# Kernel tuning notes

Measured on AMD Instinct MI355X. Metric: run time of the kernel, lower is better.

Reference implementation:

```python
import jax, jax.numpy as jnp
import numpy as np

EMBED_DIM = 1024
N_HEADS = 16
HEAD_DIM = EMBED_DIM // N_HEADS
B, S = 2, 2048


def setup_inputs() -> dict:
    key = jax.random.key(0)
    ks = jax.random.split(key, 8)
    scale = 1.0 / np.sqrt(EMBED_DIM)
    return {
        "key": jax.random.normal(ks[0], (B, S, EMBED_DIM), jnp.float32),
        "query": jax.random.normal(ks[1], (B, S, EMBED_DIM), jnp.float32),
        "value": jax.random.normal(ks[2], (B, S, EMBED_DIM), jnp.float32),
        # nn.Linear weights stored [out_features, in_features], applied as x @ W.T
        "Wq": jax.random.normal(ks[3], (EMBED_DIM, EMBED_DIM), jnp.float32) * scale,
        "Wk": jax.random.normal(ks[4], (EMBED_DIM, EMBED_DIM), jnp.float32) * scale,
        "Wv": jax.random.normal(ks[5], (EMBED_DIM, EMBED_DIM), jnp.float32) * scale,
        "Wo": jax.random.normal(ks[6], (EMBED_DIM, EMBED_DIM), jnp.float32) * scale,
        "bo": jax.random.normal(ks[7], (EMBED_DIM,), jnp.float32) * scale,
    }


def reference(key, query, value, Wq, Wk, Wv, Wo, bo) -> jnp.ndarray:
    b = key.shape[0]
    # project and split heads: [B, S, E] -> [B, H, S, D]
    def split_heads(x):
        return x.reshape(b, -1, N_HEADS, HEAD_DIM).transpose(0, 2, 1, 3)
    q = split_heads(query @ Wq.T)
    k = split_heads(key @ Wk.T)
    v = split_heads(value @ Wv.T)
    scores = jnp.einsum("bhqd,bhkd->bhqk", q, k) / np.sqrt(HEAD_DIM)
    attn = jax.nn.softmax(scores, axis=-1)
    ctx = jnp.einsum("bhqk,bhkd->bhqd", attn, v)  # [B, H, S, D]
    ctx = ctx.transpose(0, 2, 1, 3).reshape(b, -1, EMBED_DIM)
    return ctx @ Wo.T + bo
```

## Files before the change

kernel.cpp:

```cpp
#include <hip/hip_runtime.h>

typedef unsigned short u16;
typedef __bf16 bf8 __attribute__((ext_vector_type(8)));
typedef float f4 __attribute__((ext_vector_type(4)));

typedef __attribute__((address_space(1))) const unsigned int gas_u32;
typedef __attribute__((address_space(3))) unsigned int las_u32;
#define ASYNC16(g, l) __builtin_amdgcn_global_load_lds((gas_u32*)(g), (las_u32*)(l), 16, 0, 0)

__device__ __forceinline__ u16 f2bf(float f) {
    union { float f; unsigned int u; } v; v.f = f;
    return (u16)((v.u + 0x7fffu + ((v.u >> 16) & 1u)) >> 16);
}

__device__ __forceinline__ float fexp2(float x) {
#if __has_builtin(__builtin_amdgcn_exp2f)
  return __builtin_amdgcn_exp2f(x);
#else
  return __expf(x * 0.69314718056f);
#endif
}

__global__ __launch_bounds__(256) void cvt_all(
    const float* __restrict__ k_, const float* __restrict__ q_, const float* __restrict__ v_,
    const float* __restrict__ wq, const float* __restrict__ wk, const float* __restrict__ wv,
    const float* __restrict__ wo, u16* __restrict__ ws) {
  size_t e = ((size_t)blockIdx.x * 256 + threadIdx.x) * 8;
  const float* src;
  if      (e <  4194304) src = k_ + e;
  else if (e <  8388608) src = q_ + (e - 4194304);
  else if (e < 12582912) src = v_ + (e - 8388608);
  else if (e < 13631488) src = wq + (e - 12582912);
  else if (e < 14680064) src = wk + (e - 13631488);
  else if (e < 15728640) src = wv + (e - 14680064);
  else                   src = wo + (e - 15728640);
  float4 f0 = ((const float4*)src)[0];
  float4 f1 = ((const float4*)src)[1];
  uint4 o;
  o.x = (unsigned)f2bf(f0.x) | ((unsigned)f2bf(f0.y) << 16);
  o.y = (unsigned)f2bf(f0.z) | ((unsigned)f2bf(f0.w) << 16);
  o.z = (unsigned)f2bf(f1.x) | ((unsigned)f2bf(f1.y) << 16);
  o.w = (unsigned)f2bf(f1.z) | ((unsigned)f2bf(f1.w) << 16);
  *(uint4*)(ws + e) = o;
}

template<int BM, bool FINAL>
__device__ __forceinline__ void gemm_tile(const u16* __restrict__ A, const u16* __restrict__ Bm,
                                          u16* __restrict__ Cb, float* __restrict__ Cf,
                                          const float* __restrict__ bias, float scale,
                                          int bm, int bn, int ldc) {
  __shared__ u16 As[BM*32];
  __shared__ u16 Bs[128*32];
  const int tid = threadIdx.x;
  const int wave = tid >> 6, lane = tid & 63;
  const int wm = wave >> 1, wn = wave & 1;
  const int quad = lane >> 4, l16 = lane & 15;
  const int MI = BM / 32;

  f4 acc[MI][4];
  const f4 zz = {0.f, 0.f, 0.f, 0.f};
  #pragma unroll
  for (int i = 0; i < MI; i++)
    #pragma unroll
    for (int j = 0; j < 4; j++) acc[i][j] = zz;

  const u16* ga = A  + (size_t)(bm*BM  + wave*16 + (lane>>2)) * 1024 + (lane&3)*8;
  const u16* gb = Bm + (size_t)(bn*128 + wave*16 + (lane>>2)) * 1024 + (lane&3)*8;
  u16* la = As + wave*512 + lane*8;
  u16* lb = Bs + wave*512 + lane*8;

  for (int kt = 0; kt < 1024; kt += 32) {
    ASYNC16(ga, la);
    if (BM == 128) ASYNC16(ga + 64*1024, la + 2048);
    ASYNC16(gb,           lb);
    ASYNC16(gb + 64*1024, lb + 2048);
    ga += 32; gb += 32;
    __syncthreads();
    bf8 af[MI];
    #pragma unroll
    for (int mi = 0; mi < MI; mi++)
      af[mi] = *(const bf8*)(As + (wm*(BM/2) + mi*16 + l16)*32 + quad*8);
    #pragma unroll
    for (int ni = 0; ni < 4; ni++) {
      bf8 bfr = *(const bf8*)(Bs + (wn*64 + ni*16 + l16)*32 + quad*8);
      #pragma unroll
      for (int mi = 0; mi < MI; mi++)
        acc[mi][ni] = __builtin_amdgcn_mfma_f32_16x16x32_bf16(af[mi], bfr, acc[mi][ni], 0, 0, 0);
    }
    __syncthreads();
  }

  #pragma unroll
  for (int mi = 0; mi < MI; mi++)
    #pragma unroll
    for (int ni = 0; ni < 4; ni++) {
      const int col = bn*128 + wn*64 + ni*16 + l16;
      #pragma unroll
      for (int r = 0; r < 4; r++) {
        const int row = bm*BM + wm*(BM/2) + mi*16 + quad*4 + r;
        if (FINAL) Cf[(size_t)row*ldc + col] = acc[mi][ni][r] + bias[col];
        else       Cb[(size_t)row*ldc + col] = f2bf(acc[mi][ni][r] * scale);
      }
    }
}

#define QSCALE 0.180336880f

__global__ __launch_bounds__(256, 3) void gemm_qkv(
    const u16* __restrict__ xq, const u16* __restrict__ xk, const u16* __restrict__ xv,
    const u16* __restrict__ wq, const u16* __restrict__ wk, const u16* __restrict__ wv,
    u16* __restrict__ Qo, u16* __restrict__ Ko, u16* __restrict__ Vto) {
  if (blockIdx.z == 0)
    gemm_tile<128,false>(xq, wq, Qo, nullptr, nullptr, QSCALE, blockIdx.y, blockIdx.x, 1024);
  else if (blockIdx.z == 1)
    gemm_tile<128,false>(xk, wk, Ko, nullptr, nullptr, 1.0f, blockIdx.y, blockIdx.x, 1024);
  else
    gemm_tile<128,false>(wv, xv, Vto, nullptr, nullptr, 1.0f, blockIdx.x, blockIdx.y, 4096);
}

__global__ __launch_bounds__(256, 2) void gemm_out(
    const u16* __restrict__ ctx, const u16* __restrict__ wo,
    const float* __restrict__ bias, float* __restrict__ out) {
  gemm_tile<64,true>(ctx, wo, nullptr, out, bias, 1.0f, blockIdx.y, blockIdx.x, 1024);
}

__global__ __launch_bounds__(256, 3) void flash_attn(
    const u16* __restrict__ Qg, const u16* __restrict__ Kg,
    const u16* __restrict__ Vtg, u16* __restrict__ ctx) {
  __shared__ uint4 smem4[2560];
  u16* Ks = (u16*)smem4;
  u16* Vt = (u16*)smem4 + 8192;
  u16* Pt = (u16*)smem4 + 16384;
  float* Of = (float*)smem4;
  float* Lf = (float*)smem4 + 2*64*68;

  const int tid = threadIdx.x;
  const int wave = tid >> 6, lane = tid & 63;
  const int quad = lane >> 4, l16 = lane & 15;
  const int wq = wave >> 1, wk = wave & 1;
  const int qt = blockIdx.x, h = blockIdx.y, b = blockIdx.z;
  u16* Ptw = Pt + wave*1024;

  bf8 qf[2][2];
  {
    const u16* qp = Qg + (size_t)(b*2048 + qt*64 + wq*32)*1024 + h*64;
    #pragma unroll
    for (int qs = 0; qs < 2; qs++)
      #pragma unroll
      for (int kc = 0; kc < 2; kc++)
        qf[qs][kc] = *(const bf8*)(qp + (size_t)(qs*16 + l16)*1024 + kc*32 + quad*8);
  }

  const f4 zz = {0.f, 0.f, 0.f, 0.f};
  f4 ot[4][2];
  float lrow[2] = {0.f, 0.f};
  #pragma unroll
  for (int ds = 0; ds < 4; ds++)
    #pragma unroll
    for (int qs = 0; qs < 2; qs++) ot[ds][qs] = zz;

  const int kr = tid >> 3;
  const u16* kga = Kg + (size_t)(b*2048 + kr)*1024 + h*64 + ((tid & 7) ^ (kr & 7))*8;
  const int vd = tid >> 4;
  const u16* vga = Vtg + (size_t)(h*64 + vd)*4096 + b*2048 + (((tid & 15) ^ vd))*8;
  u16* kld = Ks + tid*8;
  u16* vld = Vt + tid*8;

  for (int kv0 = 0; kv0 < 2048; kv0 += 128) {
    __syncthreads();
    #pragma unroll
    for (int p = 0; p < 4; p++) ASYNC16(kga + (size_t)(kv0 + p*32)*1024, kld + p*2048);
    #pragma unroll
    for (int p = 0; p < 4; p++) ASYNC16(vga + (size_t)(p*16)*4096 + kv0, vld + p*2048);
    __syncthreads();

    #pragma unroll
    for (int kb = 0; kb < 2; kb++) {
      f4 st[2][2];
      #pragma unroll
      for (int ks = 0; ks < 2; ks++)
        #pragma unroll
        for (int qs = 0; qs < 2; qs++) st[ks][qs] = zz;
      #pragma unroll
      for (int ks = 0; ks < 2; ks++) {
        const int key = wk*64 + kb*32 + ks*16 + l16;
        #pragma unroll
        for (int kc = 0; kc < 2; kc++) {
          bf8 kf = *(const bf8*)(Ks + key*64 + (((kc*4 + quad) ^ (l16 & 7))*8));
          #pragma unroll
          for (int qs = 0; qs < 2; qs++)
            st[ks][qs] = __builtin_amdgcn_mfma_f32_16x16x32_bf16(kf, qf[qs][kc], st[ks][qs], 0, 0, 0);
        }
      }
      #pragma unroll
      for (int ks = 0; ks < 2; ks++)
        #pragma unroll
        for (int qs = 0; qs < 2; qs++) {
          float p0 = fexp2(st[ks][qs][0]), p1 = fexp2(st[ks][qs][1]);
          float p2 = fexp2(st[ks][qs][2]), p3 = fexp2(st[ks][qs][3]);
          lrow[qs] += (p0 + p1) + (p2 + p3);
          uint2 w;
          w.x = (unsigned)f2bf(p0) | ((unsigned)f2bf(p1) << 16);
          w.y = (unsigned)f2bf(p2) | ((unsigned)f2bf(p3) << 16);
          *(uint2*)(Ptw + (qs*16 + l16)*32 + (((ks*4 + quad) ^ (l16 & 7))*4)) = w;
        }
      bf8 pf[2];
      #pragma unroll
      for (int qs = 0; qs < 2; qs++) {
        uint2 a = *(const uint2*)(Ptw + (qs*16 + l16)*32 + (((quad*2 + 0) ^ (l16 & 7))*4));
        uint2 c = *(const uint2*)(Ptw + (qs*16 + l16)*32 + (((quad*2 + 1) ^ (l16 & 7))*4));
        union { uint4 u; bf8 v; } pu;
        pu.u.x = a.x; pu.u.y = a.y; pu.u.z = c.x; pu.u.w = c.y;
        pf[qs] = pu.v;
      }
      #pragma unroll
      for (int ds = 0; ds < 4; ds++) {
        const int d = ds*16 + l16;
        bf8 vf = *(const bf8*)(Vt + d*128 + (((wk*8 + kb*4 + quad) ^ l16)*8));
        #pragma unroll
        for (int qs = 0; qs < 2; qs++)
          ot[ds][qs] = __builtin_amdgcn_mfma_f32_16x16x32_bf16(vf, pf[qs], ot[ds][qs], 0, 0, 0);
      }
    }
  }

  __syncthreads();
  #pragma unroll
  for (int qs = 0; qs < 2; qs++) {
    lrow[qs] += __shfl_xor(lrow[qs], 16);
    lrow[qs] += __shfl_xor(lrow[qs], 32);
  }
  float* Ofw = Of + wk*(64*68);
  #pragma unroll
  for (int ds = 0; ds < 4; ds++)
    #pragma unroll
    for (int qs = 0; qs < 2; qs++)
      #pragma unroll
      for (int r = 0; r < 4; r++)
        Ofw[(wq*32 + qs*16 + l16)*68 + ds*16 + quad*4 + r] = ot[ds][qs][r];
  if (quad == 0) {
    Lf[wk*64 + wq*32 + l16]      = lrow[0];
    Lf[wk*64 + wq*32 + 16 + l16] = lrow[1];
  }
  __syncthreads();
  {
    const int qr = tid >> 2, dp = (tid & 3)*16;
    const float inv = 1.f / (Lf[qr] + Lf[64 + qr]);
    const float* o0 = Of + qr*68 + dp;
    const float* o1 = o0 + 64*68;
    u16 ov[16];
    #pragma unroll
    for (int i = 0; i < 16; i++) ov[i] = f2bf((o0[i] + o1[i]) * inv);
    u16* cp = ctx + (size_t)(b*2048 + qt*64 + qr)*1024 + h*64 + dp;
    *(uint4*)cp       = *(uint4*)&ov[0];
    *(uint4*)(cp + 8) = *(uint4*)&ov[8];
  }
}

extern "C" void kernel_launch(void* const* d_in, const int* in_sizes, int n_in,
                              void* d_out, int out_size, void* d_ws, size_t ws_size,
                              hipStream_t stream) {
  const float* key_  = (const float*)d_in[0];
  const float* query = (const float*)d_in[1];
  const float* value = (const float*)d_in[2];
  const float* Wq = (const float*)d_in[3];
  const float* Wk = (const float*)d_in[4];
  const float* Wv = (const float*)d_in[5];
  const float* Wo = (const float*)d_in[6];
  const float* bo = (const float*)d_in[7];
  float* out = (float*)d_out;

  u16* ws  = (u16*)d_ws;
  u16* xkb = ws;
  u16* xqb = ws + 4194304;
  u16* xvb = ws + 8388608;
  u16* Wqb = ws + 12582912;
  u16* Wkb = ws + 13631488;
  u16* Wvb = ws + 14680064;
  u16* Wob = ws + 15728640;
  u16* Qb  = ws + 16777216;
  u16* Kb  = ws + 20971520;
  u16* Vtb = ws + 25165824;
  u16* Cb  = ws + 29360128;

  cvt_all<<<8192, 256, 0, stream>>>(key_, query, value, Wq, Wk, Wv, Wo, ws);
  gemm_qkv<<<dim3(8, 32, 3), 256, 0, stream>>>(xqb, xkb, xvb, Wqb, Wkb, Wvb, Qb, Kb, Vtb);
  flash_attn<<<dim3(32, 16, 2), 256, 0, stream>>>(Qb, Kb, Vtb, Cb);
  gemm_out<<<dim3(8, 64), 256, 0, stream>>>(Cb, Wob, bo, out);
}
```

Measured before the change: 221.3 us.

## Deepen GEMM K-tile to 64 with XOR-swizzled LDS and reorder block grids

```diff
diff --git a/kernel.cpp b/kernel.cpp
--- a/kernel.cpp
+++ b/kernel.cpp
@@ -49,8 +49,8 @@
                                           u16* __restrict__ Cb, float* __restrict__ Cf,
                                           const float* __restrict__ bias, float scale,
                                           int bm, int bn, int ldc) {
-  __shared__ u16 As[BM*32];
-  __shared__ u16 Bs[128*32];
+  __shared__ u16 As[BM*64];
+  __shared__ u16 Bs[128*64];
   const int tid = threadIdx.x;
   const int wave = tid >> 6, lane = tid & 63;
   const int wm = wave >> 1, wn = wave & 1;
@@ -64,28 +64,32 @@
     #pragma unroll
     for (int j = 0; j < 4; j++) acc[i][j] = zz;
 
-  const u16* ga = A  + (size_t)(bm*BM  + wave*16 + (lane>>2)) * 1024 + (lane&3)*8;
-  const u16* gb = Bm + (size_t)(bn*128 + wave*16 + (lane>>2)) * 1024 + (lane&3)*8;
-  u16* la = As + wave*512 + lane*8;
-  u16* lb = Bs + wave*512 + lane*8;
-
-  for (int kt = 0; kt < 1024; kt += 32) {
-    ASYNC16(ga, la);
-    if (BM == 128) ASYNC16(ga + 64*1024, la + 2048);
-    ASYNC16(gb,           lb);
-    ASYNC16(gb + 64*1024, lb + 2048);
-    ga += 32; gb += 32;
-    __syncthreads();
-    bf8 af[MI];
-    #pragma unroll
-    for (int mi = 0; mi < MI; mi++)
-      af[mi] = *(const bf8*)(As + (wm*(BM/2) + mi*16 + l16)*32 + quad*8);
-    #pragma unroll
-    for (int ni = 0; ni < 4; ni++) {
-      bf8 bfr = *(const bf8*)(Bs + (wn*64 + ni*16 + l16)*32 + quad*8);
+  const int kr = tid >> 3;
+  const int cs = (tid & 7) ^ (kr & 7);
+  const u16* ga = A  + (size_t)(bm*BM  + kr)*1024 + cs*8;
+  const u16* gb = Bm + (size_t)(bn*128 + kr)*1024 + cs*8;
+  u16* la = As + tid*8;
+  u16* lb = Bs + tid*8;
+
+  for (int kt = 0; kt < 1024; kt += 64) {
+    #pragma unroll
+    for (int p = 0; p < BM/32; p++) ASYNC16(ga + (size_t)(p*32)*1024 + kt, la + p*2048);
+    #pragma unroll
+    for (int p = 0; p < 4; p++)     ASYNC16(gb + (size_t)(p*32)*1024 + kt, lb + p*2048);
+    __syncthreads();
+    #pragma unroll
+    for (int kk = 0; kk < 2; kk++) {
+      bf8 af[MI];
       #pragma unroll
       for (int mi = 0; mi < MI; mi++)
-        acc[mi][ni] = __builtin_amdgcn_mfma_f32_16x16x32_bf16(af[mi], bfr, acc[mi][ni], 0, 0, 0);
+        af[mi] = *(const bf8*)(As + (wm*(BM/2) + mi*16 + l16)*64 + (((kk*4 + quad) ^ (l16 & 7))*8));
+      #pragma unroll
+      for (int ni = 0; ni < 4; ni++) {
+        bf8 bfr = *(const bf8*)(Bs + (wn*64 + ni*16 + l16)*64 + (((kk*4 + quad) ^ (l16 & 7))*8));
+        #pragma unroll
+        for (int mi = 0; mi < MI; mi++)
+          acc[mi][ni] = __builtin_amdgcn_mfma_f32_16x16x32_bf16(af[mi], bfr, acc[mi][ni], 0, 0, 0);
+      }
     }
     __syncthreads();
   }
@@ -111,17 +115,17 @@
     const u16* __restrict__ wq, const u16* __restrict__ wk, const u16* __restrict__ wv,
     u16* __restrict__ Qo, u16* __restrict__ Ko, u16* __restrict__ Vto) {
   if (blockIdx.z == 0)
-    gemm_tile<128,false>(xq, wq, Qo, nullptr, nullptr, QSCALE, blockIdx.y, blockIdx.x, 1024);
+    gemm_tile<128,false>(xq, wq, Qo, nullptr, nullptr, QSCALE, blockIdx.x, blockIdx.y, 1024);
   else if (blockIdx.z == 1)
-    gemm_tile<128,false>(xk, wk, Ko, nullptr, nullptr, 1.0f, blockIdx.y, blockIdx.x, 1024);
+    gemm_tile<128,false>(xk, wk, Ko, nullptr, nullptr, 1.0f, blockIdx.x, blockIdx.y, 1024);
   else
-    gemm_tile<128,false>(wv, xv, Vto, nullptr, nullptr, 1.0f, blockIdx.x, blockIdx.y, 4096);
+    gemm_tile<128,false>(wv, xv, Vto, nullptr, nullptr, 1.0f, blockIdx.y, blockIdx.x, 4096);
 }
 
 __global__ __launch_bounds__(256, 2) void gemm_out(
     const u16* __restrict__ ctx, const u16* __restrict__ wo,
     const float* __restrict__ bias, float* __restrict__ out) {
-  gemm_tile<64,true>(ctx, wo, nullptr, out, bias, 1.0f, blockIdx.y, blockIdx.x, 1024);
+  gemm_tile<64,true>(ctx, wo, nullptr, out, bias, 1.0f, blockIdx.x, blockIdx.y, 1024);
 }
 
 __global__ __launch_bounds__(256, 3) void flash_attn(
@@ -138,7 +142,7 @@
   const int wave = tid >> 6, lane = tid & 63;
   const int quad = lane >> 4, l16 = lane & 15;
   const int wq = wave >> 1, wk = wave & 1;
-  const int qt = blockIdx.x, h = blockIdx.y, b = blockIdx.z;
+  const int h = blockIdx.x, qt = blockIdx.y, b = blockIdx.z;
   u16* Ptw = Pt + wave*1024;
 
   bf8 qf[2][2];
@@ -284,7 +288,7 @@
   u16* Cb  = ws + 29360128;
 
   cvt_all<<<8192, 256, 0, stream>>>(key_, query, value, Wq, Wk, Wv, Wo, ws);
-  gemm_qkv<<<dim3(8, 32, 3), 256, 0, stream>>>(xqb, xkb, xvb, Wqb, Wkb, Wvb, Qb, Kb, Vtb);
-  flash_attn<<<dim3(32, 16, 2), 256, 0, stream>>>(Qb, Kb, Vtb, Cb);
-  gemm_out<<<dim3(8, 64), 256, 0, stream>>>(Cb, Wob, bo, out);
-}
+  gemm_qkv<<<dim3(32, 8, 3), 256, 0, stream>>>(xqb, xkb, xvb, Wqb, Wkb, Wvb, Qb, Kb, Vtb);
+  flash_attn<<<dim3(16, 32, 2), 256, 0, stream>>>(Qb, Kb, Vtb, Cb);
+  gemm_out<<<dim3(64, 8), 256, 0, stream>>>(Cb, Wob, bo, out);
+}
```

New measurement: 213.3 us. -3.6%, faster.
